# Optimization experiments

Hardware: AMD Instinct MI355X
Metric: run time of the kernel (lower is better)

The kernel has to match this reference:

```python
import jax, jax.numpy as jnp
import numpy as np
from jax import lax

T_SCALE = 100
D_SCALE = 100
NUM_SAMPLE = 32
PER_BIN = 3
RATIO = 0.5


def _build_sample_mask(tscale=T_SCALE, dscale=D_SCALE, num_sample=NUM_SAMPLE, perbin=PER_BIN, ratio=RATIO):
    # Vectorized, bit-faithful port of BM_layer._get_interp1d_mask (incl. np.modf
    # semantics matching math.modf for negative samples).
    T, D = tscale, dscale
    total = num_sample * perbin
    s = np.arange(T, dtype=np.float64)[:, None, None]   # start index
    d = np.arange(D, dtype=np.float64)[None, :, None]   # duration index
    clen = d + 1.0
    xmin = s - ratio * clen
    plen = d + 2.0 * ratio * clen                        # sample_xmax - sample_xmin
    step = plen / (total - 1.0)
    ii = np.arange(total, dtype=np.float64)[None, None, :]
    samples = xmin + step * ii                           # [T_start, D, total]
    frac, down_f = np.modf(samples)                      # trunc-toward-zero, like math.modf
    down = down_f.astype(np.int64)
    up = np.ceil(samples).astype(np.int64)
    acc = np.zeros((T, D, num_sample, T), dtype=np.float64)  # [start, dur, bin, time]
    S, Dg, I = np.indices((T, D, total))
    Bn = I // perbin
    m = (down >= 0) & (down <= T - 1)
    np.add.at(acc, (S[m], Dg[m], Bn[m], down[m]), 1.0 - frac[m])
    m = (up >= 0) & (up <= T - 1)
    np.add.at(acc, (S[m], Dg[m], Bn[m], up[m]), frac[m])
    acc /= perbin
    valid = (np.arange(T)[:, None] + np.arange(D)[None, :]) < T  # start+dur < tscale
    acc *= valid[:, :, None, None]
    # torch layout: [time, sample, dur, start]
    return jnp.asarray(acc.transpose(3, 2, 1, 0).astype(np.float32))


def _conv2d(x, w, pad):
    return lax.conv_general_dilated(x, w, (1, 1), ((pad, pad), (pad, pad)),
                                    dimension_numbers=('NCHW', 'OIHW', 'NCHW'))


def setup_inputs() -> dict:
    key = jax.random.key(0)
    ks = jax.random.split(key, 8)
    B, C_in, T = 4, 256, T_SCALE

    def w(k, shape, fan_in):
        return jax.random.normal(k, shape, dtype=jnp.float32) * (1.0 / np.sqrt(fan_in))

    return {
        'x': jax.random.normal(ks[0], (B, C_in, T), dtype=jnp.float32),
        'w_rd': w(ks[1], (128, C_in, 3), C_in * 3),      'b_rd': jnp.zeros((128,), jnp.float32),
        'w3d': w(ks[2], (512, 128, NUM_SAMPLE), 128 * NUM_SAMPLE), 'b3d': jnp.zeros((512,), jnp.float32),
        'w2d': w(ks[3], (128, 512), 512),                 'b2d': jnp.zeros((128,), jnp.float32),
        'wf1': w(ks[4], (128, 128, 3, 3), 128 * 9),       'bf1': jnp.zeros((128,), jnp.float32),
        'wf2': w(ks[5], (128, 128, 3, 3), 128 * 9),       'bf2': jnp.zeros((128,), jnp.float32),
        'wf3': w(ks[6], (2, 128), 128),                   'bf3': jnp.zeros((2,), jnp.float32),
        'sample_mask': _build_sample_mask(),
    }


def reference(x, w_rd, b_rd, w3d, b3d, w2d, b2d, wf1, bf1, wf2, bf2, wf3, bf3, sample_mask):
    # reduce_dim: Conv1d(256->128, k=3, pad=1) + ReLU
    h = lax.conv_general_dilated(x, w_rd, (1,), ((1, 1),),
                                 dimension_numbers=('NCH', 'OIH', 'NCH'))
    h = jax.nn.relu(h + b_rd[None, :, None])                       # [B,128,T]
    # tensordot over time axis against fixed interpolation mask
    map_base = jnp.einsum('bct,tsdu->bcsdu', h, sample_mask)       # [B,128,32,D,T]
    # conv3d with kernel (32,1,1) stride (32,1,1) == contraction over (c, s)
    m3 = jax.nn.relu(jnp.einsum('bcsdu,ocs->bodu', map_base, w3d) + b3d[None, :, None, None])
    # 1x1 conv2d 512->128
    m2 = jax.nn.relu(jnp.einsum('bodu,ko->bkdu', m3, w2d) + b2d[None, :, None, None])
    # PEM.fc head
    f = jax.nn.relu(_conv2d(m2, wf1, 1) + bf1[None, :, None, None])
    f = jax.nn.relu(_conv2d(f, wf2, 1) + bf2[None, :, None, None])
    out = jax.nn.sigmoid(jnp.einsum('bchw,kc->bkhw', f, wf3) + bf3[None, :, None, None])
    return out  # [B, 2, D, T]
```

## Files before the change

kernel.cpp:

```cpp
#include <hip/hip_runtime.h>
#include <hip/hip_bf16.h>
#include <cstdint>
#include <cstddef>

static constexpr int B   = 4;
static constexpr int CIN = 256;
static constexpr int T   = 100;
static constexpr int D   = 100;
static constexpr int S   = 32;
static constexpr int C1  = 128;
static constexpr int DU  = D * T;

typedef __attribute__((ext_vector_type(8))) short bfv8;
typedef __attribute__((ext_vector_type(4))) float fx4;
typedef unsigned short us;

static __device__ __forceinline__ unsigned short f2bf(float f) {
    unsigned int x = __float_as_uint(f);
    x += 0x7FFFu + ((x >> 16) & 1u);
    return (unsigned short)(x >> 16);
}
static __device__ __forceinline__ unsigned int pk2(float a, float b) {
    return (unsigned int)f2bf(a) | ((unsigned int)f2bf(b) << 16);
}

#define MFMA16(A, Bq, C) __builtin_amdgcn_mfma_f32_16x16x32_bf16((A), (Bq), (C), 0, 0, 0)

static __device__ __forceinline__ void gload16(const void* g, void* l) {
    __builtin_amdgcn_global_load_lds(
        (const __attribute__((address_space(1))) void*)g,
        (__attribute__((address_space(3))) void*)l, 16, 0, 0);
}

__global__ void kPrep(const float* __restrict__ w3d, us* __restrict__ w3B,
                      const float* __restrict__ w2d, us* __restrict__ w2b,
                      const float* __restrict__ wf1, us* __restrict__ wfb1,
                      const float* __restrict__ wf2, us* __restrict__ wfb2) {
    int bid = blockIdx.x;
    int t = threadIdx.x;
    if (bid < 8192) {
        int tid = bid * 256 + t;
        int c = tid & 127;
        int o = (tid >> 7) & 511;
        int s = tid >> 16;
        w3B[tid] = f2bf(w3d[(o * 128 + c) * 32 + s]);
    } else if (bid < 8448) {
        int tid = (bid - 8192) * 256 + t;
        w2b[tid] = f2bf(w2d[tid]);
    } else if (bid < 9024) {
        int tid = (bid - 8448) * 256 + t;
        int c   = tid & 127;
        int k   = (tid >> 7) & 127;
        int tap = tid >> 14;
        wfb1[tid] = f2bf(wf1[(size_t)(k * 128 + c) * 9 + tap]);
    } else {
        int tid = (bid - 9024) * 256 + t;
        int c   = tid & 127;
        int k   = (tid >> 7) & 127;
        int tap = tid >> 14;
        wfb2[tid] = f2bf(wf2[(size_t)(k * 128 + c) * 9 + tap]);
    }
}

__global__ void kConv1d(const float* __restrict__ x, const float* __restrict__ wrd,
                        const float* __restrict__ brd, us* __restrict__ hT) {
    __shared__ float wl[CIN * 3];
    int b = blockIdx.x >> 7;
    int o = blockIdx.x & 127;
    for (int i = threadIdx.x; i < CIN * 3; i += blockDim.x)
        wl[i] = wrd[o * CIN * 3 + i];
    __syncthreads();
    int t = threadIdx.x;
    float val = 0.f;
    if (t < T) {
        float acc = brd[o];
        const float* xb = x + (size_t)b * CIN * T;
        for (int c = 0; c < CIN; ++c) {
            float xm = (t > 0)     ? xb[c * T + t - 1] : 0.f;
            float x0 =               xb[c * T + t];
            float xp = (t < T - 1) ? xb[c * T + t + 1] : 0.f;
            acc = fmaf(wl[c * 3 + 0], xm, acc);
            acc = fmaf(wl[c * 3 + 1], x0, acc);
            acc = fmaf(wl[c * 3 + 2], xp, acc);
        }
        val = fmaxf(acc, 0.f);
    }
    hT[((size_t)b * 128 + t) * 128 + o] = f2bf(val);
}

__global__ __launch_bounds__(256, 2)
void kQm(const us* __restrict__ w3B, const us* __restrict__ hT,
         us* __restrict__ QT) {
    int bid = blockIdx.x;
    int oh = bid & 1;
    int s  = (bid >> 1) & 31;
    int b  = bid >> 6;
    int tid = threadIdx.x;
    int w   = tid >> 6;
    int l   = tid & 63;
    int l15 = l & 15, lg = l >> 4;
    int obase = oh * 256 + w * 64;
    fx4 acc[4][8];
#pragma unroll
    for (int m = 0; m < 4; ++m)
#pragma unroll
        for (int n = 0; n < 8; ++n) acc[m][n] = (fx4){0.f, 0.f, 0.f, 0.f};

#pragma unroll
    for (int ks = 0; ks < 4; ++ks) {
        int kofs = ks * 32 + lg * 8;
        bfv8 a0 = *(const bfv8*)(w3B + (size_t)(s * 512 + obase + 0 * 16 + l15) * 128 + kofs);
        bfv8 a1 = *(const bfv8*)(w3B + (size_t)(s * 512 + obase + 1 * 16 + l15) * 128 + kofs);
        bfv8 a2 = *(const bfv8*)(w3B + (size_t)(s * 512 + obase + 2 * 16 + l15) * 128 + kofs);
        bfv8 a3 = *(const bfv8*)(w3B + (size_t)(s * 512 + obase + 3 * 16 + l15) * 128 + kofs);
#pragma unroll
        for (int n = 0; n < 8; ++n) {
            bfv8 bq = *(const bfv8*)(hT + (size_t)(b * 128 + n * 16 + l15) * 128 + kofs);
            acc[0][n] = MFMA16(a0, bq, acc[0][n]);
            acc[1][n] = MFMA16(a1, bq, acc[1][n]);
            acc[2][n] = MFMA16(a2, bq, acc[2][n]);
            acc[3][n] = MFMA16(a3, bq, acc[3][n]);
        }
    }
    us* outb = QT + (size_t)(b * 32 + s) * 512 * 128;
#pragma unroll
    for (int m = 0; m < 4; ++m)
#pragma unroll
        for (int n = 0; n < 8; ++n)
#pragma unroll
            for (int r = 0; r < 4; ++r) {
                int o = obase + m * 16 + lg * 4 + r;
                outb[(size_t)o * 128 + n * 16 + l15] = f2bf(acc[m][n][r]);
            }
}

__global__ __launch_bounds__(128, 4)
void kMaskW(const float* __restrict__ mask, us* __restrict__ maskW) {
    int bid = blockIdx.x;
    int ut = bid % 7;
    int dp = (bid / 7) % 50;
    int s  = bid / 350;
    int tid = threadIdx.x;
    int di = tid >> 6;
    int l  = tid & 63;
    int l15 = l & 15, lg = l >> 4;
    int u0 = ut * 16;
    int d0 = dp * 2;

    float step0 = (2.f * d0 + 1.f) * (1.f / 95.f);
    float step1 = (2.f * d0 + 3.f) * (1.f / 95.f);
    float xoff0 = -0.5f * (d0 + 1.f);
    float xoff1 = -0.5f * (d0 + 2.f);
    float fs = (float)(3 * s);
    float f0 = xoff0 + fs * step0;
    float f1 = xoff1 + fs * step1;
    float pminT = (float)u0 + fminf(f0, f1);
    float pmaxT = (float)(u0 + 15) + fmaxf(f0 + 2.f * step0, f1 + 2.f * step1);
    bool skip = (pminT > 100.01f) || (pmaxT < -1.01f);
    int t0 = (int)floorf(pminT) - 1;
    if (t0 < 0) t0 = 0;
    t0 &= ~7;
    if (t0 > 96) t0 = 96;

    int u = u0 + l15;
    int d = d0 + di;
    float v[8];
#pragma unroll
    for (int j = 0; j < 8; ++j) {
        int t = t0 + lg * 8 + j;
        v[j] = 0.f;
        if (!skip && t < 100 && u < 100)
            v[j] = mask[(((size_t)t * 32 + s) * 100 + d) * 100 + u];
    }
    uint4 pk;
    pk.x = pk2(v[0], v[1]); pk.y = pk2(v[2], v[3]);
    pk.z = pk2(v[4], v[5]); pk.w = pk2(v[6], v[7]);
    *(uint4*)(maskW + (size_t)bid * 1024 + tid * 8) = pk;
}

__global__ __launch_bounds__(128, 8)
void kM3m(const us* __restrict__ maskW, const us* __restrict__ QT,
          const float* __restrict__ b3d, us* __restrict__ m3b) {
    __shared__ int sl[32];
    __shared__ int nsh;
    int bid = blockIdx.x;
    int x  = bid & 7;
    int b  = x >> 1;
    int oh = x & 1;
    int i  = bid >> 3;
    int dp = i / 14;
    int r  = i % 14;
    int ut = r >> 1;
    int wsel = r & 1;
    int u0 = ut * 16;
    int d0 = dp * 2;
    int tid = threadIdx.x;
    int w   = tid >> 6;
    int l   = tid & 63;
    int l15 = l & 15, lg = l >> 4;
    int obase = oh * 256 + wsel * 128 + w * 64;

    if (tid < 64) {
        int s = tid;
        float step0 = (2.f * d0 + 1.f) * (1.f / 95.f);
        float step1 = (2.f * d0 + 3.f) * (1.f / 95.f);
        float xoff0 = -0.5f * (d0 + 1.f);
        float xoff1 = -0.5f * (d0 + 2.f);
        float fs = (float)(3 * s);
        float f0 = xoff0 + fs * step0;
        float f1 = xoff1 + fs * step1;
        float pminT = (float)u0 + fminf(f0, f1);
        float pmaxT = (float)(u0 + 15) + fmaxf(f0 + 2.f * step0, f1 + 2.f * step1);
        bool valid = (s < 32) && !((pminT > 100.01f) || (pmaxT < -1.01f));
        int t0 = (int)floorf(pminT) - 1;
        if (t0 < 0) t0 = 0;
        t0 &= ~7;
        if (t0 > 96) t0 = 96;
        unsigned long long mb = __ballot(valid);
        int rank = __popcll(mb & ((1ull << tid) - 1ull));
        if (valid) sl[rank] = (t0 << 8) | s;
        if (tid == 0) nsh = (int)__popcll(mb);
    }
    __syncthreads();
    int ns = nsh;

    fx4 acc0[4], acc1[4];
#pragma unroll
    for (int n = 0; n < 4; ++n) {
        acc0[n] = (fx4){0.f, 0.f, 0.f, 0.f};
        acc1[n] = (fx4){0.f, 0.f, 0.f, 0.f};
    }

    const us* QTb = QT + (size_t)b * 32 * 65536
                       + (size_t)(obase + l15) * 128 + lg * 8;
    const us* mwBase = maskW + (size_t)(dp * 7 + ut) * 1024 + l * 8;

    for (int si = 0; si < ns; ++si) {
        int pk = sl[si];
        int s_ = pk & 255, t0_ = pk >> 8;
        const us* mw = mwBase + (size_t)s_ * (350 * 1024);
        bfv8 A0 = *(const bfv8*)mw;
        bfv8 A1 = *(const bfv8*)(mw + 512);
        const us* qs = QTb + (size_t)s_ * 65536 + t0_;
        bfv8 B0 = *(const bfv8*)(qs);
        bfv8 B1 = *(const bfv8*)(qs + 2048);
        bfv8 B2 = *(const bfv8*)(qs + 4096);
        bfv8 B3 = *(const bfv8*)(qs + 6144);
        __builtin_amdgcn_s_setprio(1);
        acc0[0] = MFMA16(A0, B0, acc0[0]);  acc1[0] = MFMA16(A1, B0, acc1[0]);
        acc0[1] = MFMA16(A0, B1, acc0[1]);  acc1[1] = MFMA16(A1, B1, acc1[1]);
        acc0[2] = MFMA16(A0, B2, acc0[2]);  acc1[2] = MFMA16(A1, B2, acc1[2]);
        acc0[3] = MFMA16(A0, B3, acc0[3]);  acc1[3] = MFMA16(A1, B3, acc1[3]);
        __builtin_amdgcn_s_setprio(0);
    }

#pragma unroll
    for (int n = 0; n < 4; ++n) {
        int o = obase + n * 16 + l15;
        float bias = b3d[o];
#pragma unroll
        for (int r4 = 0; r4 < 4; ++r4) {
            int u = u0 + lg * 4 + r4;
            if (u < 100) {
                m3b[((size_t)b * DU + d0 * 100 + u) * 512 + o] =
                    f2bf(fmaxf(acc0[n][r4] + bias, 0.f));
                m3b[((size_t)b * DU + (d0 + 1) * 100 + u) * 512 + o] =
                    f2bf(fmaxf(acc1[n][r4] + bias, 0.f));
            }
        }
    }
}

__global__ __launch_bounds__(256, 4)
void kM2m(const us* __restrict__ m3b, const us* __restrict__ w2b,
          const float* __restrict__ b2d, us* __restrict__ m2b) {
    int blk  = blockIdx.x;
    int tile = blk % 157;
    int b    = blk / 157;
    int du0  = tile * 64;
    int tid = threadIdx.x;
    int w   = tid >> 6;
    int l   = tid & 63;
    int l15 = l & 15, lg = l >> 4;
    fx4 acc[8];
#pragma unroll
    for (int n = 0; n < 8; ++n) acc[n] = (fx4){0.f, 0.f, 0.f, 0.f};

    int dua = du0 + w * 16 + l15; if (dua > 9999) dua = 9999;
    const us* ap = m3b + ((size_t)b * DU + dua) * 512;
#pragma unroll 4
    for (int ks = 0; ks < 16; ++ks) {
        bfv8 a = *(const bfv8*)(ap + ks * 32 + lg * 8);
#pragma unroll
        for (int n = 0; n < 8; ++n) {
            bfv8 bq = *(const bfv8*)(w2b + (size_t)(n * 16 + l15) * 512 + ks * 32 + lg * 8);
            acc[n] = MFMA16(a, bq, acc[n]);
        }
    }
#pragma unroll
    for (int n = 0; n < 8; ++n) {
        int k = n * 16 + l15;
        float bias = b2d[k];
#pragma unroll
        for (int r = 0; r < 4; ++r) {
            int du = du0 + w * 16 + lg * 4 + r;
            if (du < DU)
                m2b[((size_t)b * DU + du) * 128 + k] = f2bf(fmaxf(acc[n][r] + bias, 0.f));
        }
    }
}

template<int HEAD>
__global__ __launch_bounds__(256, 2)
void kConvM(const us* __restrict__ fin, const us* __restrict__ wfb,
            const float* __restrict__ bf, us* __restrict__ fout,
            const float* __restrict__ wf3, const float* __restrict__ bf3,
            float* __restrict__ hout) {
    __shared__ us slab[6 * 18 * 128];
    __shared__ us wl2[2][8192];
    int blk = blockIdx.x;
    int ut = blk % 7;
    int dt = (blk / 7) % 25;
    int b  = blk / 175;
    int u0 = ut * 16, d0 = dt * 4;
    int tid = threadIdx.x;
    int w   = tid >> 6;
    int l   = tid & 63;
    int l15 = l & 15, lg = l >> 4;
    fx4 acc[8];
#pragma unroll
    for (int n = 0; n < 8; ++n) acc[n] = (fx4){0.f, 0.f, 0.f, 0.f};

#define STAGE_W(BUF, P)                                                        \
    {   const int tap_ = (P) >> 1, ch_ = (P) & 1;                              \
        const us* wsrc = wfb + (size_t)tap_ * 16384 + ch_ * 64;                \
        _Pragma("unroll")                                                      \
        for (int rr = 0; rr < 4; ++rr) {                                       \
            int seg = rr * 4 + w;                                              \
            int off = seg * 1024 + l * 16;                                     \
            int k_ = off >> 7, cb_ = off & 127;                                \
            int cbs = cb_ ^ ((k_ & 7) << 4);                                   \
            gload16(wsrc + (size_t)k_ * 128 + (cbs >> 1),                      \
                    (char*)&wl2[BUF][0] + seg * 1024);                         \
        }                                                                      \
    }

    for (int i = tid; i < 1728; i += 256) {
        int cc = i & 15;
        int uu = (i >> 4) % 18;
        int dd = (i >> 4) / 18;
        int dr = d0 - 1 + dd, su = u0 - 1 + uu;
        uint4 v = {0u, 0u, 0u, 0u};
        if (dr >= 0 && dr < 100 && su >= 0 && su < 100)
            v = *(const uint4*)(fin + ((size_t)b * DU + dr * 100 + su) * 128 + cc * 8);
        int byte = (dd * 18 + uu) * 256 + ((cc * 16) ^ ((uu & 7) << 4));
        *(uint4*)((char*)slab + byte) = v;
    }
    STAGE_W(0, 0)
    __syncthreads();

#pragma unroll
    for (int p = 0; p < 18; ++p) {
        if (p + 1 < 18) STAGE_W((p + 1) & 1, p + 1)
        const int tap = p >> 1, ch = p & 1;
        const int dy = tap / 3, dx = tap % 3;
        int uu = l15 + dx;
        int ddr = w + dy;
        int arow = (ddr * 18 + uu) * 256;
        int aswz = (uu & 7) << 4;
        const char* wbuf = (const char*)&wl2[p & 1][0];
#pragma unroll
        for (int cs = 0; cs < 2; ++cs) {
            int cbyte = ch * 128 + cs * 64 + lg * 16;
            bfv8 a = *(const bfv8*)((const char*)slab + arow + (cbyte ^ aswz));
            int wcb = cs * 64 + lg * 16;
#pragma unroll
            for (int n = 0; n < 8; ++n) {
                int k = n * 16 + l15;
                bfv8 bq = *(const bfv8*)(wbuf + k * 128 + (wcb ^ ((k & 7) << 4)));
                acc[n] = MFMA16(a, bq, acc[n]);
            }
        }
        __syncthreads();
    }
#undef STAGE_W

    int d = d0 + w;
    if (HEAD == 0) {
#pragma unroll
        for (int n = 0; n < 8; ++n) {
            int k = n * 16 + l15;
            float bias = bf[k];
#pragma unroll
            for (int r = 0; r < 4; ++r) {
                int u = u0 + lg * 4 + r;
                if (u < 100)
                    fout[((size_t)b * DU + d * 100 + u) * 128 + k] =
                        f2bf(fmaxf(acc[n][r] + bias, 0.f));
            }
        }
    } else {
#pragma unroll
        for (int r = 0; r < 4; ++r) {
            float p0 = 0.f, p1 = 0.f;
#pragma unroll
            for (int n = 0; n < 8; ++n) {
                int k = n * 16 + l15;
                float f = fmaxf(acc[n][r] + bf[k], 0.f);
                p0 = fmaf(f, wf3[k], p0);
                p1 = fmaf(f, wf3[128 + k], p1);
            }
            p0 += __shfl_xor(p0, 1); p0 += __shfl_xor(p0, 2);
            p0 += __shfl_xor(p0, 4); p0 += __shfl_xor(p0, 8);
            p1 += __shfl_xor(p1, 1); p1 += __shfl_xor(p1, 2);
            p1 += __shfl_xor(p1, 4); p1 += __shfl_xor(p1, 8);
            int u = u0 + lg * 4 + r;
            if (l15 == 0 && u < 100) {
                int du = d * 100 + u;
                hout[((size_t)b * 2 + 0) * DU + du] = 1.f / (1.f + expf(-(p0 + bf3[0])));
                hout[((size_t)b * 2 + 1) * DU + du] = 1.f / (1.f + expf(-(p1 + bf3[1])));
            }
        }
    }
}

extern "C" void kernel_launch(void* const* d_in, const int* in_sizes, int n_in,
                              void* d_out, int out_size, void* d_ws, size_t ws_size,
                              hipStream_t stream) {
    const float* x    = (const float*)d_in[0];
    const float* wrd  = (const float*)d_in[1];
    const float* brd  = (const float*)d_in[2];
    const float* w3d  = (const float*)d_in[3];
    const float* b3d  = (const float*)d_in[4];
    const float* w2d  = (const float*)d_in[5];
    const float* b2d  = (const float*)d_in[6];
    const float* wf1  = (const float*)d_in[7];
    const float* bf1  = (const float*)d_in[8];
    const float* wf2  = (const float*)d_in[9];
    const float* bf2  = (const float*)d_in[10];
    const float* wf3  = (const float*)d_in[11];
    const float* bf3  = (const float*)d_in[12];
    const float* mask = (const float*)d_in[13];

    float* ws = (float*)d_ws;
    us* hT    = (us*)(ws + 0);
    us* w3B   = (us*)(ws + 32768);
    us* w2b   = (us*)(ws + 1081344);
    us* wfb1  = (us*)(ws + 1114112);
    us* wfb2  = (us*)(ws + 1187840);
    us* QT    = (us*)(ws + 1261568);
    us* maskW = (us*)(ws + 5455872);
    us* m2b   = (us*)(ws + 5455872);
    us* f1b   = (us*)(ws + 8015872);
    us* m3b   = (us*)(ws + 11190272);

    kPrep<<<9600, 256, 0, stream>>>(w3d, w3B, w2d, w2b, wf1, wfb1, wf2, wfb2);
    kConv1d<<<B * C1, 128, 0, stream>>>(x, wrd, brd, hT);
    kMaskW<<<11200, 128, 0, stream>>>(mask, maskW);
    kQm<<<256, 256, 0, stream>>>(w3B, hT, QT);
    kM3m<<<5600, 128, 0, stream>>>(maskW, QT, b3d, m3b);
    kM2m<<<B * 157, 256, 0, stream>>>(m3b, w2b, b2d, m2b);
    kConvM<0><<<B * 25 * 7, 256, 0, stream>>>(m2b, wfb1, bf1, f1b,
                                              nullptr, nullptr, nullptr);
    kConvM<1><<<B * 25 * 7, 256, 0, stream>>>(f1b, wfb2, bf2, nullptr,
                                              wf3, bf3, (float*)d_out);
}
```

Before: 344.2 us.

## Tile kM3m over four durations per block to reuse QT loads

The kM3m contraction now covers four duration rows per block instead of two, so each pair of QT B-fragment loads feeds 16 MFMAs instead of 8 and the grid shrinks to half as many blocks. kMaskW is reshaped to emit 4-row mask tiles, and the time window start is aligned to 4 rather than 8, which needs split 8-byte loads for the B operand. The union window over four durations is wider, so fewer samples may be skipped, and register pressure rises with 16 accumulators.

```diff
diff --git a/kernel.cpp b/kernel.cpp
--- a/kernel.cpp
+++ b/kernel.cpp
@@ -12,6 +12,7 @@
 static constexpr int DU  = D * T;
 
 typedef __attribute__((ext_vector_type(8))) short bfv8;
+typedef __attribute__((ext_vector_type(4))) short bfv4;
 typedef __attribute__((ext_vector_type(4))) float fx4;
 typedef unsigned short us;
 
@@ -134,36 +135,39 @@
             }
 }
 
-__global__ __launch_bounds__(128, 4)
+__global__ __launch_bounds__(256, 4)
 void kMaskW(const float* __restrict__ mask, us* __restrict__ maskW) {
     int bid = blockIdx.x;
     int ut = bid % 7;
-    int dp = (bid / 7) % 50;
-    int s  = bid / 350;
+    int dq = (bid / 7) % 25;
+    int s  = bid / 175;
     int tid = threadIdx.x;
-    int di = tid >> 6;
+    int dd = tid >> 6;
     int l  = tid & 63;
     int l15 = l & 15, lg = l >> 4;
     int u0 = ut * 16;
-    int d0 = dp * 2;
-
-    float step0 = (2.f * d0 + 1.f) * (1.f / 95.f);
-    float step1 = (2.f * d0 + 3.f) * (1.f / 95.f);
-    float xoff0 = -0.5f * (d0 + 1.f);
-    float xoff1 = -0.5f * (d0 + 2.f);
-    float fs = (float)(3 * s);
-    float f0 = xoff0 + fs * step0;
-    float f1 = xoff1 + fs * step1;
-    float pminT = (float)u0 + fminf(f0, f1);
-    float pmaxT = (float)(u0 + 15) + fmaxf(f0 + 2.f * step0, f1 + 2.f * step1);
+    int d0 = dq * 4;
+
+    float fs1 = (float)(3 * s), fs2 = (float)(3 * s + 2);
+    float pmin = 1e30f, pmax = -1e30f;
+#pragma unroll
+    for (int j = 0; j < 4; ++j) {
+        float dj = (float)(d0 + j);
+        float step = (2.f * dj + 1.f) * (1.f / 95.f);
+        float xoff = -0.5f * (dj + 1.f);
+        pmin = fminf(pmin, xoff + fs1 * step);
+        pmax = fmaxf(pmax, xoff + fs2 * step);
+    }
+    float pminT = (float)u0 + pmin;
+    float pmaxT = (float)(u0 + 15) + pmax;
     bool skip = (pminT > 100.01f) || (pmaxT < -1.01f);
     int t0 = (int)floorf(pminT) - 1;
     if (t0 < 0) t0 = 0;
-    t0 &= ~7;
+    t0 &= ~3;
     if (t0 > 96) t0 = 96;
 
     int u = u0 + l15;
-    int d = d0 + di;
+    int d = d0 + dd;
     float v[8];
 #pragma unroll
     for (int j = 0; j < 8; ++j) {
@@ -175,10 +179,10 @@
     uint4 pk;
     pk.x = pk2(v[0], v[1]); pk.y = pk2(v[2], v[3]);
     pk.z = pk2(v[4], v[5]); pk.w = pk2(v[6], v[7]);
-    *(uint4*)(maskW + (size_t)bid * 1024 + tid * 8) = pk;
-}
-
-__global__ __launch_bounds__(128, 8)
+    *(uint4*)(maskW + (size_t)bid * 2048 + tid * 8) = pk;
+}
+
+__global__ __launch_bounds__(128, 4)
 void kM3m(const us* __restrict__ maskW, const us* __restrict__ QT,
           const float* __restrict__ b3d, us* __restrict__ m3b) {
     __shared__ int sl[32];
@@ -186,35 +190,38 @@
     int bid = blockIdx.x;
     int x  = bid & 7;
     int b  = x >> 1;
-    int oh = x & 1;
+    int ohalf = x & 1;
     int i  = bid >> 3;
-    int dp = i / 14;
-    int r  = i % 14;
-    int ut = r >> 1;
-    int wsel = r & 1;
+    int dq = i / 14;
+    int r2 = i % 14;
+    int ut = r2 >> 1;
+    int os = r2 & 1;
     int u0 = ut * 16;
-    int d0 = dp * 2;
+    int d0 = dq * 4;
     int tid = threadIdx.x;
     int w   = tid >> 6;
     int l   = tid & 63;
     int l15 = l & 15, lg = l >> 4;
-    int obase = oh * 256 + wsel * 128 + w * 64;
+    int obase = ohalf * 256 + os * 128 + w * 64;
 
     if (tid < 64) {
         int s = tid;
-        float step0 = (2.f * d0 + 1.f) * (1.f / 95.f);
-        float step1 = (2.f * d0 + 3.f) * (1.f / 95.f);
-        float xoff0 = -0.5f * (d0 + 1.f);
-        float xoff1 = -0.5f * (d0 + 2.f);
-        float fs = (float)(3 * s);
-        float f0 = xoff0 + fs * step0;
-        float f1 = xoff1 + fs * step1;
-        float pminT = (float)u0 + fminf(f0, f1);
-        float pmaxT = (float)(u0 + 15) + fmaxf(f0 + 2.f * step0, f1 + 2.f * step1);
+        float fs1 = (float)(3 * s), fs2 = (float)(3 * s + 2);
+        float pmin = 1e30f, pmax = -1e30f;
+#pragma unroll
+        for (int j = 0; j < 4; ++j) {
+            float dj = (float)(d0 + j);
+            float step = (2.f * dj + 1.f) * (1.f / 95.f);
+            float xoff = -0.5f * (dj + 1.f);
+            pmin = fminf(pmin, xoff + fs1 * step);
+            pmax = fmaxf(pmax, xoff + fs2 * step);
+        }
+        float pminT = (float)u0 + pmin;
+        float pmaxT = (float)(u0 + 15) + pmax;
         bool valid = (s < 32) && !((pminT > 100.01f) || (pmaxT < -1.01f));
         int t0 = (int)floorf(pminT) - 1;
         if (t0 < 0) t0 = 0;
-        t0 &= ~7;
+        t0 &= ~3;
         if (t0 > 96) t0 = 96;
         unsigned long long mb = __ballot(valid);
         int rank = __popcll(mb & ((1ull << tid) - 1ull));
@@ -224,48 +231,57 @@
     __syncthreads();
     int ns = nsh;
 
-    fx4 acc0[4], acc1[4];
-#pragma unroll
-    for (int n = 0; n < 4; ++n) {
-        acc0[n] = (fx4){0.f, 0.f, 0.f, 0.f};
-        acc1[n] = (fx4){0.f, 0.f, 0.f, 0.f};
-    }
+    fx4 acc[4][4];
+#pragma unroll
+    for (int m = 0; m < 4; ++m)
+#pragma unroll
+        for (int n = 0; n < 4; ++n) acc[m][n] = (fx4){0.f, 0.f, 0.f, 0.f};
 
     const us* QTb = QT + (size_t)b * 32 * 65536
                        + (size_t)(obase + l15) * 128 + lg * 8;
-    const us* mwBase = maskW + (size_t)(dp * 7 + ut) * 1024 + l * 8;
+    const us* mwBase = maskW + (size_t)(dq * 7 + ut) * 2048 + l * 8;
 
     for (int si = 0; si < ns; ++si) {
         int pk = sl[si];
         int s_ = pk & 255, t0_ = pk >> 8;
-        const us* mw = mwBase + (size_t)s_ * (350 * 1024);
-        bfv8 A0 = *(const bfv8*)mw;
+        const us* mw = mwBase + (size_t)s_ * 358400;
+        bfv8 A0 = *(const bfv8*)(mw);
         bfv8 A1 = *(const bfv8*)(mw + 512);
+        bfv8 A2 = *(const bfv8*)(mw + 1024);
+        bfv8 A3 = *(const bfv8*)(mw + 1536);
         const us* qs = QTb + (size_t)s_ * 65536 + t0_;
-        bfv8 B0 = *(const bfv8*)(qs);
-        bfv8 B1 = *(const bfv8*)(qs + 2048);
-        bfv8 B2 = *(const bfv8*)(qs + 4096);
-        bfv8 B3 = *(const bfv8*)(qs + 6144);
+        bfv4 b0l = *(const bfv4*)(qs);        bfv4 b0h = *(const bfv4*)(qs + 4);
+        bfv4 b1l = *(const bfv4*)(qs + 2048); bfv4 b1h = *(const bfv4*)(qs + 2052);
+        bfv4 b2l = *(const bfv4*)(qs + 4096); bfv4 b2h = *(const bfv4*)(qs + 4100);
+        bfv4 b3l = *(const bfv4*)(qs + 6144); bfv4 b3h = *(const bfv4*)(qs + 6148);
+        bfv8 B0 = __builtin_shufflevector(b0l, b0h, 0, 1, 2, 3, 4, 5, 6, 7);
+        bfv8 B1 = __builtin_shufflevector(b1l, b1h, 0, 1, 2, 3, 4, 5, 6, 7);
+        bfv8 B2 = __builtin_shufflevector(b2l, b2h, 0, 1, 2, 3, 4, 5, 6, 7);
+        bfv8 B3 = __builtin_shufflevector(b3l, b3h, 0, 1, 2, 3, 4, 5, 6, 7);
         __builtin_amdgcn_s_setprio(1);
-        acc0[0] = MFMA16(A0, B0, acc0[0]);  acc1[0] = MFMA16(A1, B0, acc1[0]);
-        acc0[1] = MFMA16(A0, B1, acc0[1]);  acc1[1] = MFMA16(A1, B1, acc1[1]);
-        acc0[2] = MFMA16(A0, B2, acc0[2]);  acc1[2] = MFMA16(A1, B2, acc1[2]);
-        acc0[3] = MFMA16(A0, B3, acc0[3]);  acc1[3] = MFMA16(A1, B3, acc1[3]);
+        acc[0][0] = MFMA16(A0, B0, acc[0][0]);  acc[1][0] = MFMA16(A1, B0, acc[1][0]);
+        acc[2][0] = MFMA16(A2, B0, acc[2][0]);  acc[3][0] = MFMA16(A3, B0, acc[3][0]);
+        acc[0][1] = MFMA16(A0, B1, acc[0][1]);  acc[1][1] = MFMA16(A1, B1, acc[1][1]);
+        acc[2][1] = MFMA16(A2, B1, acc[2][1]);  acc[3][1] = MFMA16(A3, B1, acc[3][1]);
+        acc[0][2] = MFMA16(A0, B2, acc[0][2]);  acc[1][2] = MFMA16(A1, B2, acc[1][2]);
+        acc[2][2] = MFMA16(A2, B2, acc[2][2]);  acc[3][2] = MFMA16(A3, B2, acc[3][2]);
+        acc[0][3] = MFMA16(A0, B3, acc[0][3]);  acc[1][3] = MFMA16(A1, B3, acc[1][3]);
+        acc[2][3] = MFMA16(A2, B3, acc[2][3]);  acc[3][3] = MFMA16(A3, B3, acc[3][3]);
         __builtin_amdgcn_s_setprio(0);
     }
 
 #pragma unroll
-    for (int n = 0; n < 4; ++n) {
-        int o = obase + n * 16 + l15;
-        float bias = b3d[o];
-#pragma unroll
-        for (int r4 = 0; r4 < 4; ++r4) {
-            int u = u0 + lg * 4 + r4;
-            if (u < 100) {
-                m3b[((size_t)b * DU + d0 * 100 + u) * 512 + o] =
-                    f2bf(fmaxf(acc0[n][r4] + bias, 0.f));
-                m3b[((size_t)b * DU + (d0 + 1) * 100 + u) * 512 + o] =
-                    f2bf(fmaxf(acc1[n][r4] + bias, 0.f));
+    for (int dd = 0; dd < 4; ++dd) {
+#pragma unroll
+        for (int n = 0; n < 4; ++n) {
+            int o = obase + n * 16 + l15;
+            float bias = b3d[o];
+#pragma unroll
+            for (int r4 = 0; r4 < 4; ++r4) {
+                int u = u0 + lg * 4 + r4;
+                if (u < 100)
+                    m3b[((size_t)b * DU + (d0 + dd) * 100 + u) * 512 + o] =
+                        f2bf(fmaxf(acc[dd][n][r4] + bias, 0.f));
             }
         }
     }
@@ -456,9 +472,9 @@
 
     kPrep<<<9600, 256, 0, stream>>>(w3d, w3B, w2d, w2b, wf1, wfb1, wf2, wfb2);
     kConv1d<<<B * C1, 128, 0, stream>>>(x, wrd, brd, hT);
-    kMaskW<<<11200, 128, 0, stream>>>(mask, maskW);
+    kMaskW<<<5600, 256, 0, stream>>>(mask, maskW);
     kQm<<<256, 256, 0, stream>>>(w3B, hT, QT);
-    kM3m<<<5600, 128, 0, stream>>>(maskW, QT, b3d, m3b);
+    kM3m<<<2800, 128, 0, stream>>>(maskW, QT, b3d, m3b);
     kM2m<<<B * 157, 256, 0, stream>>>(m3b, w2b, b2d, m2b);
     kConvM<0><<<B * 25 * 7, 256, 0, stream>>>(m2b, wfb1, bf1, f1b,
                                               nullptr, nullptr, nullptr);
```

Measured after the change: 298.6 us. 13.2% less time.
